# Kernel tuning notes

Measured on AMD Instinct MI355X. Metric: run time of the kernel, lower is better.

## Reference

```python
import jax, jax.numpy as jnp
import numpy as np


def setup_inputs() -> dict:
    key = jax.random.key(0)
    ks = jax.random.split(key, 6)
    B, S, D, E, F, C = 4, 2048, 1024, 8, 4096, 512
    return {
        "x": jax.random.normal(ks[0], (B, S, D), dtype=jnp.float32),
        "router": jax.random.normal(ks[1], (D, E), dtype=jnp.float32) * (1.0 / np.sqrt(D)),
        "w1": jax.random.normal(ks[2], (E, D, F), dtype=jnp.float32) * (1.0 / np.sqrt(D)),
        "b1": jnp.zeros((E, F), dtype=jnp.float32),
        "w2": jax.random.normal(ks[3], (E, F, D), dtype=jnp.float32) * (1.0 / np.sqrt(F)),
        "b2": jnp.zeros((E, D), dtype=jnp.float32),
        "capacity": C,
    }


def reference(x, router, w1, b1, w2, b2, capacity):
    # x: (B,S,D); router: (D,E); per-expert FFN weights stacked on E.
    B, S, D = x.shape
    # Gate: softmax over experts, then each expert picks its top-C tokens.
    logits = jnp.einsum('bsd,de->bse', x, router)            # (B,S,E)
    affinity = jax.nn.softmax(logits, axis=-1)               # (B,S,E)
    gating, index = jax.lax.top_k(jnp.transpose(affinity, (0, 2, 1)), capacity)  # (B,E,C)
    # Dispatch: gather token features per (expert, slot). Equivalent to the
    # one-hot einsum 'becs,bsd->becd' in the original (same math, true gather).
    x_in = jax.vmap(lambda xb, ib: xb[ib])(x, index)         # (B,E,C,D)
    # Per-expert GPT2 FFN: Linear -> GELU -> Linear (grouped GEMMs over E).
    h = jax.nn.gelu(jnp.einsum('becd,edf->becf', x_in, w1) + b1[None, :, None, :],
                    approximate=False)                        # (B,E,C,F)
    x_e = jnp.einsum('becf,efd->becd', h, w2) + b2[None, :, None, :]  # (B,E,C,D)
    # Combine: weighted scatter-add back to token positions. Equivalent to
    # einsum 'becs,bec,becd->bsd' with the one-hot dispatch mask.
    weighted = gating[..., None] * x_e                       # (B,E,C,D)
    out = jax.vmap(
        lambda ib, vb: jnp.zeros((S, D), x.dtype).at[ib.reshape(-1)].add(vb.reshape(-1, D))
    )(index, weighted)                                       # (B,S,D)
    return out
```

## Files before the change

### kernel.cpp

```cpp
#include <hip/hip_runtime.h>
#include <hip/hip_bf16.h>

#define B_ 4
#define S_ 2048
#define D_ 1024
#define E_ 8
#define F_ 4096
#define C_ 512
#define BE_ (B_*E_)

typedef __attribute__((ext_vector_type(8))) short bf16x8;
typedef __attribute__((ext_vector_type(4))) float f32x4;
typedef unsigned short u16;

static constexpr size_t OFF_AFF  = 0;
static constexpr size_t OFF_IDX  = 262144;
static constexpr size_t OFF_GATE = 327680;
static constexpr size_t OFF_XIN  = 393216;
static constexpr size_t OFF_WT1  = OFF_XIN + (size_t)BE_*C_*D_*2;
static constexpr size_t OFF_WT2  = OFF_WT1 + (size_t)E_*F_*D_*2;
static constexpr size_t OFF_H    = OFF_WT2 + (size_t)E_*D_*F_*2;
static constexpr size_t WS_NEED  = OFF_H   + (size_t)BE_*C_*F_*2;

static __device__ __forceinline__ u16 f2bf(float x) {
  __hip_bfloat16 h = __float2bfloat16(x);
  return *reinterpret_cast<u16*>(&h);
}

static __device__ __forceinline__ void gload16(const void* g, void* l) {
  __builtin_amdgcn_global_load_lds(
      (const __attribute__((address_space(1))) unsigned int*)g,
      (__attribute__((address_space(3))) unsigned int*)l, 16, 0, 0);
}

__global__ void router_kernel(const float* __restrict__ x,
                              const float* __restrict__ router,
                              float* __restrict__ aff) {
  int t = blockIdx.x;
  int b = t / S_, s = t % S_;
  int lane = threadIdx.x;
  const float* xrow = x + (size_t)t * D_;
  float acc[E_];
#pragma unroll
  for (int e = 0; e < E_; ++e) acc[e] = 0.f;
  for (int i = 0; i < D_/64; ++i) {
    int d = lane + i*64;
    float xv = xrow[d];
    const float* r = router + (size_t)d * E_;
#pragma unroll
    for (int e = 0; e < E_; ++e) acc[e] += xv * r[e];
  }
#pragma unroll
  for (int e = 0; e < E_; ++e) {
    float v = acc[e];
    for (int off = 32; off; off >>= 1) v += __shfl_down(v, off);
    acc[e] = v;
  }
  if (lane == 0) {
    float mx = acc[0];
#pragma unroll
    for (int e = 1; e < E_; ++e) mx = fmaxf(mx, acc[e]);
    float ev[E_]; float sum = 0.f;
#pragma unroll
    for (int e = 0; e < E_; ++e) { ev[e] = expf(acc[e] - mx); sum += ev[e]; }
    float inv = 1.0f / sum;
#pragma unroll
    for (int e = 0; e < E_; ++e) aff[((size_t)(b*E_ + e))*S_ + s] = ev[e]*inv;
  }
}

__global__ void topk_kernel(const float* __restrict__ aff,
                            int* __restrict__ idxb, float* __restrict__ gateb) {
  __shared__ unsigned long long keys[S_];
  int be = blockIdx.x;
  const float* a = aff + (size_t)be * S_;
  int tid = threadIdx.x;
  for (int i = tid; i < S_; i += 1024) {
    unsigned vb = __float_as_uint(a[i]);
    keys[i] = ((unsigned long long)(~vb) << 32) | (unsigned)i;
  }
  __syncthreads();
  for (int k = 2; k <= S_; k <<= 1) {
    for (int j = k >> 1; j > 0; j >>= 1) {
      for (int i = tid; i < S_; i += 1024) {
        int ixj = i ^ j;
        if (ixj > i) {
          unsigned long long ka = keys[i], kb = keys[ixj];
          bool up = ((i & k) == 0);
          if ((ka > kb) == up) { keys[i] = kb; keys[ixj] = ka; }
        }
      }
      __syncthreads();
    }
  }
  for (int c = tid; c < C_; c += 1024) {
    unsigned long long kk = keys[c];
    idxb[be*C_ + c]  = (int)(kk & 0xffffffffu);
    gateb[be*C_ + c] = __uint_as_float(~(unsigned)(kk >> 32));
  }
}

__global__ void gather_kernel(const float* __restrict__ x,
                              const int* __restrict__ idxb,
                              u16* __restrict__ x_in) {
  int rid = blockIdx.x;
  int be = rid >> 9;
  int b = be >> 3;
  int tok = idxb[rid];
  const float4* src = (const float4*)(x + ((size_t)(b * S_ + tok)) * D_);
  ushort4* dst = (ushort4*)(x_in + (size_t)rid * D_);
  int t = threadIdx.x;
#pragma unroll
  for (int i = 0; i < 2; ++i) {
    float4 v = src[t + i*128];
    ushort4 o;
    o.x = f2bf(v.x); o.y = f2bf(v.y); o.z = f2bf(v.z); o.w = f2bf(v.w);
    dst[t + i*128] = o;
  }
}

__global__ void trans_kernel(const float* __restrict__ src,
                             u16* __restrict__ dst, int RI, int RJ) {
  __shared__ float t[64][65];
  int e  = blockIdx.z;
  int j0 = blockIdx.x * 64;
  int i0 = blockIdx.y * 64;
  const float* s = src + (size_t)e * RI * RJ;
  u16* d = dst + (size_t)e * RI * RJ;
  int tid = threadIdx.x;
#pragma unroll
  for (int it = 0; it < 4; ++it) {
    int fid = it*256 + tid;
    int r = fid >> 4, c4 = fid & 15;
    float4 v = *(const float4*)(s + (size_t)(i0 + r) * RJ + j0 + c4*4);
    t[r][c4*4+0] = v.x; t[r][c4*4+1] = v.y; t[r][c4*4+2] = v.z; t[r][c4*4+3] = v.w;
  }
  __syncthreads();
#pragma unroll
  for (int it = 0; it < 4; ++it) {
    int fid = it*256 + tid;
    int rn = fid >> 4, c4 = fid & 15;
    ushort4 o;
    o.x = f2bf(t[c4*4+0][rn]); o.y = f2bf(t[c4*4+1][rn]);
    o.z = f2bf(t[c4*4+2][rn]); o.w = f2bf(t[c4*4+3][rn]);
    *(ushort4*)(d + (size_t)(j0 + rn) * RI + i0 + c4*4) = o;
  }
}

template<int EPI, int N, int K, int NBLK>
__global__ __launch_bounds__(256, 4)
void gemm_kernel(const u16* __restrict__ A, const u16* __restrict__ Bt,
                 const float* __restrict__ bias, void* __restrict__ outp,
                 const int* __restrict__ idxb, const float* __restrict__ gateb,
                 float* __restrict__ dout) {
  __shared__ __align__(16) char lds[32768];
  char* ldsA = lds;
  char* ldsB = lds + 16384;
  const int tid  = threadIdx.x;
  const int wave = tid >> 6, lane = tid & 63;

  const int bid = blockIdx.x;
  const int e   = bid & 7;
  const int r   = bid >> 3;
  const int nb  = r % NBLK;
  const int rm  = r / NBLK;
  const int mb  = rm & 3;
  const int b   = rm >> 2;
  const int be  = b * E_ + e;
  const int m0  = mb * 128;
  const int n0  = nb * 128;

  const u16* Ab = A  + (size_t)be * C_ * K + (size_t)m0 * K;
  const u16* Bb = Bt + (size_t)e  * N  * K + (size_t)n0 * K;

  f32x4 acc[4][4];
#pragma unroll
  for (int i = 0; i < 4; ++i)
#pragma unroll
    for (int j = 0; j < 4; ++j) acc[i][j] = (f32x4){0.f,0.f,0.f,0.f};

  const int wr = wave >> 1, wc = wave & 1;
  const int chi = lane >> 4;
  const int l15 = lane & 15;

  for (int kt = 0; kt < K/64; ++kt) {
    const int k0 = kt * 64;
#pragma unroll
    for (int i = 0; i < 4; ++i) {
      int slot = i*256 + tid;
      int row = slot >> 3, c = slot & 7;
      int sc = (c ^ (row & 7)) << 3;
      gload16(Ab + (size_t)row * K + k0 + sc, ldsA + (i*256 + wave*64)*16);
      gload16(Bb + (size_t)row * K + k0 + sc, ldsB + (i*256 + wave*64)*16);
    }
    __syncthreads();
    bf16x8 af[2][4], bfr[2][4];
#pragma unroll
    for (int kk = 0; kk < 2; ++kk) {
#pragma unroll
      for (int mi = 0; mi < 4; ++mi) {
        int row = wr*64 + mi*16 + l15;
        int ch  = kk*4 + chi;
        af[kk][mi] = *(const bf16x8*)(ldsA + row*128 + (((ch ^ (row & 7)) << 4)));
        int rowb = wc*64 + mi*16 + l15;
        bfr[kk][mi] = *(const bf16x8*)(ldsB + rowb*128 + (((ch ^ (rowb & 7)) << 4)));
      }
    }
#pragma unroll
    for (int kk = 0; kk < 2; ++kk)
#pragma unroll
      for (int mi = 0; mi < 4; ++mi)
#pragma unroll
        for (int ni = 0; ni < 4; ++ni)
          acc[mi][ni] = __builtin_amdgcn_mfma_f32_16x16x32_bf16(
              af[kk][mi], bfr[kk][ni], acc[mi][ni], 0, 0, 0);
    __syncthreads();
  }

  const int r4 = lane >> 4;
  if (EPI == 0) {
    __hip_bfloat16* hb = (__hip_bfloat16*)outp + (size_t)be * C_ * N;
    const float* bias_e = bias + e * N;
#pragma unroll
    for (int mi = 0; mi < 4; ++mi) {
#pragma unroll
      for (int j = 0; j < 4; ++j) {
        int row = m0 + wr*64 + mi*16 + r4*4 + j;
        __hip_bfloat16* hrow = hb + (size_t)row * N;
#pragma unroll
        for (int ni = 0; ni < 4; ++ni) {
          int col = n0 + wc*64 + ni*16 + l15;
          float v = acc[mi][ni][j] + bias_e[col];
          float g = 0.5f * v * (1.0f + erff(v * 0.70710678118654752f));
          hrow[col] = __float2bfloat16(g);
        }
      }
    }
  } else {
    const float* bias_e = bias + e * N;
    int bb = be >> 3;
#pragma unroll
    for (int mi = 0; mi < 4; ++mi) {
#pragma unroll
      for (int j = 0; j < 4; ++j) {
        int rowl = m0 + wr*64 + mi*16 + r4*4 + j;
        int tok = idxb[be*C_ + rowl];
        float gt = gateb[be*C_ + rowl];
        float* orow = dout + ((size_t)bb * S_ + tok) * (size_t)D_;
#pragma unroll
        for (int ni = 0; ni < 4; ++ni) {
          int col = n0 + wc*64 + ni*16 + l15;
          float v = (acc[mi][ni][j] + bias_e[col]) * gt;
          atomicAdd(orow + col, v);
        }
      }
    }
  }
}

extern "C" void kernel_launch(void* const* d_in, const int* in_sizes, int n_in,
                              void* d_out, int out_size, void* d_ws, size_t ws_size,
                              hipStream_t stream) {
  const float* x      = (const float*)d_in[0];
  const float* router = (const float*)d_in[1];
  const float* w1     = (const float*)d_in[2];
  const float* b1     = (const float*)d_in[3];
  const float* w2     = (const float*)d_in[4];
  const float* b2     = (const float*)d_in[5];
  float* out = (float*)d_out;

  if (ws_size < WS_NEED) return;

  char* ws = (char*)d_ws;
  float* aff   = (float*)(ws + OFF_AFF);
  int*   idxb  = (int*)(ws + OFF_IDX);
  float* gateb = (float*)(ws + OFF_GATE);
  u16*   x_in  = (u16*)(ws + OFF_XIN);
  u16*   wt1   = (u16*)(ws + OFF_WT1);
  u16*   wt2   = (u16*)(ws + OFF_WT2);
  u16*   h     = (u16*)(ws + OFF_H);

  router_kernel<<<B_*S_, 64, 0, stream>>>(x, router, aff);
  topk_kernel<<<BE_, 1024, 0, stream>>>(aff, idxb, gateb);
  gather_kernel<<<BE_*C_, 128, 0, stream>>>(x, idxb, x_in);
  trans_kernel<<<dim3(F_/64, D_/64, E_), 256, 0, stream>>>(w1, wt1, D_, F_);
  trans_kernel<<<dim3(D_/64, F_/64, E_), 256, 0, stream>>>(w2, wt2, F_, D_);
  hipMemsetAsync(d_out, 0, (size_t)out_size * sizeof(float), stream);

  gemm_kernel<0, F_, D_, F_/128><<<E_*(F_/128)*4*B_, 256, 0, stream>>>(
      x_in, wt1, b1, (void*)h, nullptr, nullptr, nullptr);
  gemm_kernel<1, D_, F_, D_/128><<<E_*(D_/128)*4*B_, 256, 0, stream>>>(
      h, wt2, b2, nullptr, idxb, gateb, out);
}
```

Before: 483.9 us.

## Rewrite expert GEMMs as 256x256 8-wave double-buffered pipelined kernel

Replaces the 128x128 single-buffered GEMM with a 256x256-tile, 512-thread kernel that uses 128KB of LDS for double buffering. Global-to-LDS loads for the next K tiles are interleaved with four MFMA phases, and manual waitcnt, barriers and setprio are used to overlap memory with compute. The larger tile raises arithmetic intensity per LDS byte and hides load latency. In exchange it lowers occupancy, leaves fewer blocks for the D-output GEMM (256 blocks), and relies on fragile hand-tuned synchronisation.

```diff
diff --git a/kernel.cpp b/kernel.cpp
--- a/kernel.cpp
+++ b/kernel.cpp
@@ -12,6 +12,8 @@
 typedef __attribute__((ext_vector_type(8))) short bf16x8;
 typedef __attribute__((ext_vector_type(4))) float f32x4;
 typedef unsigned short u16;
+
+#define MFMA16 __builtin_amdgcn_mfma_f32_16x16x32_bf16
 
 static constexpr size_t OFF_AFF  = 0;
 static constexpr size_t OFF_IDX  = 262144;
@@ -148,88 +150,164 @@
 }
 
 template<int EPI, int N, int K, int NBLK>
-__global__ __launch_bounds__(256, 4)
-void gemm_kernel(const u16* __restrict__ A, const u16* __restrict__ Bt,
-                 const float* __restrict__ bias, void* __restrict__ outp,
-                 const int* __restrict__ idxb, const float* __restrict__ gateb,
-                 float* __restrict__ dout) {
-  __shared__ __align__(16) char lds[32768];
-  char* ldsA = lds;
-  char* ldsB = lds + 16384;
+__global__ __launch_bounds__(512, 2)
+void gemm8_kernel(const u16* __restrict__ A, const u16* __restrict__ Bt,
+                  const float* __restrict__ bias, void* __restrict__ outp,
+                  const int* __restrict__ idxb, const float* __restrict__ gateb,
+                  float* __restrict__ dout) {
+  constexpr int NT = K / 64;
+  __shared__ __align__(16) char lds[131072];
   const int tid  = threadIdx.x;
   const int wave = tid >> 6, lane = tid & 63;
+  const int wm = wave >> 2, wn = wave & 3;
+  const int l15 = lane & 15, chi = lane >> 4;
 
   const int bid = blockIdx.x;
   const int e   = bid & 7;
   const int r   = bid >> 3;
   const int nb  = r % NBLK;
   const int rm  = r / NBLK;
-  const int mb  = rm & 3;
-  const int b   = rm >> 2;
+  const int mb  = rm & 1;
+  const int b   = rm >> 1;
   const int be  = b * E_ + e;
-  const int m0  = mb * 128;
-  const int n0  = nb * 128;
-
-  const u16* Ab = A  + (size_t)be * C_ * K + (size_t)m0 * K;
-  const u16* Bb = Bt + (size_t)e  * N  * K + (size_t)n0 * K;
-
-  f32x4 acc[4][4];
-#pragma unroll
-  for (int i = 0; i < 4; ++i)
+  const int m0  = mb * 256;
+  const int n0  = nb * 256;
+
+  const u16* Ab  = A  + (size_t)be * C_ * K + (size_t)m0 * K;
+  const u16* Bb  = Bt + (size_t)e  * N  * K + (size_t)n0 * K;
+  const u16* Ab2 = Ab + (size_t)128 * K;
+  const u16* Bb2 = Bb + (size_t)128 * K;
+
+  const int sr = tid >> 3, scn = tid & 7;
+  const size_t off0 = (size_t)sr * K + (size_t)((scn ^ (sr & 7)) << 3);
+  const size_t off1 = off0 + (size_t)64 * K;
+  const int ldsd = tid * 16;
+
+#define STAGE(tt, so, gb) \
+  if ((tt) < NT) { \
+    const u16* g_ = (gb) + (size_t)(tt) * 64; \
+    char* l_ = lds + (((tt) & 1) * 65536) + (so); \
+    gload16(g_ + off0, l_ + ldsd); \
+    gload16(g_ + off1, l_ + 8192 + ldsd); \
+  }
+
+  const int q7  = l15 & 7;
+  const int ch0 = ((chi    ) ^ q7) << 4;
+  const int ch1 = ((4 + chi) ^ q7) << 4;
+  const int aoff = wm * 16384 + l15 * 128;
+  const int boff = 32768 + (wn >> 1) * 16384 + (wn & 1) * 8192 + l15 * 128;
+
+  f32x4 acc[8][4];
+#pragma unroll
+  for (int i = 0; i < 8; ++i)
 #pragma unroll
     for (int j = 0; j < 4; ++j) acc[i][j] = (f32x4){0.f,0.f,0.f,0.f};
 
-  const int wr = wave >> 1, wc = wave & 1;
-  const int chi = lane >> 4;
-  const int l15 = lane & 15;
-
-  for (int kt = 0; kt < K/64; ++kt) {
-    const int k0 = kt * 64;
-#pragma unroll
-    for (int i = 0; i < 4; ++i) {
-      int slot = i*256 + tid;
-      int row = slot >> 3, c = slot & 7;
-      int sc = (c ^ (row & 7)) << 3;
-      gload16(Ab + (size_t)row * K + k0 + sc, ldsA + (i*256 + wave*64)*16);
-      gload16(Bb + (size_t)row * K + k0 + sc, ldsB + (i*256 + wave*64)*16);
-    }
-    __syncthreads();
-    bf16x8 af[2][4], bfr[2][4];
-#pragma unroll
-    for (int kk = 0; kk < 2; ++kk) {
-#pragma unroll
-      for (int mi = 0; mi < 4; ++mi) {
-        int row = wr*64 + mi*16 + l15;
-        int ch  = kk*4 + chi;
-        af[kk][mi] = *(const bf16x8*)(ldsA + row*128 + (((ch ^ (row & 7)) << 4)));
-        int rowb = wc*64 + mi*16 + l15;
-        bfr[kk][mi] = *(const bf16x8*)(ldsB + rowb*128 + (((ch ^ (rowb & 7)) << 4)));
-      }
-    }
-#pragma unroll
-    for (int kk = 0; kk < 2; ++kk)
-#pragma unroll
-      for (int mi = 0; mi < 4; ++mi)
-#pragma unroll
-        for (int ni = 0; ni < 4; ++ni)
-          acc[mi][ni] = __builtin_amdgcn_mfma_f32_16x16x32_bf16(
-              af[kk][mi], bfr[kk][ni], acc[mi][ni], 0, 0, 0);
-    __syncthreads();
-  }
+  STAGE(0, 0,     Ab);
+  STAGE(0, 16384, Ab2);
+  STAGE(0, 32768, Bb);
+  STAGE(0, 49152, Bb2);
+  STAGE(1, 32768, Bb);
+  STAGE(1, 49152, Bb2);
+  asm volatile("s_waitcnt vmcnt(4)" ::: "memory");
+  __builtin_amdgcn_s_barrier();
+
+  bf16x8 af[2][4], bA[2][2], bB[2][2];
+  for (int t = 0; t < NT; ++t) {
+    const char* cb = lds + (t & 1) * 65536;
+#pragma unroll
+    for (int m = 0; m < 4; ++m) {
+      af[0][m] = *(const bf16x8*)(cb + aoff + m*2048 + ch0);
+      af[1][m] = *(const bf16x8*)(cb + aoff + m*2048 + ch1);
+    }
+#pragma unroll
+    for (int n = 0; n < 2; ++n) {
+      bA[0][n] = *(const bf16x8*)(cb + boff + n*2048 + ch0);
+      bA[1][n] = *(const bf16x8*)(cb + boff + n*2048 + ch1);
+    }
+    STAGE(t+1, 0, Ab);
+    asm volatile("s_waitcnt lgkmcnt(8)" ::: "memory");
+    __builtin_amdgcn_s_barrier();
+    asm volatile("s_waitcnt lgkmcnt(0)" ::: "memory");
+    __builtin_amdgcn_s_setprio(1);
+#pragma unroll
+    for (int m = 0; m < 4; ++m)
+#pragma unroll
+      for (int n = 0; n < 2; ++n) {
+        acc[m][n] = MFMA16(af[0][m], bA[0][n], acc[m][n], 0, 0, 0);
+        acc[m][n] = MFMA16(af[1][m], bA[1][n], acc[m][n], 0, 0, 0);
+      }
+    __builtin_amdgcn_s_setprio(0);
+    __builtin_amdgcn_s_barrier();
+#pragma unroll
+    for (int n = 0; n < 2; ++n) {
+      bB[0][n] = *(const bf16x8*)(cb + boff + (2+n)*2048 + ch0);
+      bB[1][n] = *(const bf16x8*)(cb + boff + (2+n)*2048 + ch1);
+    }
+    STAGE(t+1, 16384, Ab2);
+    __builtin_amdgcn_s_barrier();
+    asm volatile("s_waitcnt lgkmcnt(0)" ::: "memory");
+    __builtin_amdgcn_s_setprio(1);
+#pragma unroll
+    for (int m = 0; m < 4; ++m)
+#pragma unroll
+      for (int n = 0; n < 2; ++n) {
+        acc[m][2+n] = MFMA16(af[0][m], bB[0][n], acc[m][2+n], 0, 0, 0);
+        acc[m][2+n] = MFMA16(af[1][m], bB[1][n], acc[m][2+n], 0, 0, 0);
+      }
+    __builtin_amdgcn_s_setprio(0);
+    __builtin_amdgcn_s_barrier();
+#pragma unroll
+    for (int m = 0; m < 4; ++m) {
+      af[0][m] = *(const bf16x8*)(cb + aoff + (4+m)*2048 + ch0);
+      af[1][m] = *(const bf16x8*)(cb + aoff + (4+m)*2048 + ch1);
+    }
+    STAGE(t+2, 32768, Bb);
+    __builtin_amdgcn_s_barrier();
+    asm volatile("s_waitcnt lgkmcnt(0)" ::: "memory");
+    __builtin_amdgcn_s_setprio(1);
+#pragma unroll
+    for (int m = 0; m < 4; ++m)
+#pragma unroll
+      for (int n = 0; n < 2; ++n) {
+        acc[4+m][2+n] = MFMA16(af[0][m], bB[0][n], acc[4+m][2+n], 0, 0, 0);
+        acc[4+m][2+n] = MFMA16(af[1][m], bB[1][n], acc[4+m][2+n], 0, 0, 0);
+      }
+    __builtin_amdgcn_s_setprio(0);
+    __builtin_amdgcn_s_barrier();
+    STAGE(t+2, 49152, Bb2);
+    if (t < NT-2) {
+      asm volatile("s_waitcnt vmcnt(4)" ::: "memory");
+    } else if (t == NT-2) {
+      asm volatile("s_waitcnt vmcnt(0)" ::: "memory");
+    }
+    __builtin_amdgcn_s_barrier();
+    __builtin_amdgcn_s_setprio(1);
+#pragma unroll
+    for (int m = 0; m < 4; ++m)
+#pragma unroll
+      for (int n = 0; n < 2; ++n) {
+        acc[4+m][n] = MFMA16(af[0][m], bA[0][n], acc[4+m][n], 0, 0, 0);
+        acc[4+m][n] = MFMA16(af[1][m], bA[1][n], acc[4+m][n], 0, 0, 0);
+      }
+    __builtin_amdgcn_s_setprio(0);
+    __builtin_amdgcn_s_barrier();
+  }
+#undef STAGE
 
   const int r4 = lane >> 4;
   if (EPI == 0) {
     __hip_bfloat16* hb = (__hip_bfloat16*)outp + (size_t)be * C_ * N;
     const float* bias_e = bias + e * N;
 #pragma unroll
-    for (int mi = 0; mi < 4; ++mi) {
+    for (int mi = 0; mi < 8; ++mi) {
 #pragma unroll
       for (int j = 0; j < 4; ++j) {
-        int row = m0 + wr*64 + mi*16 + r4*4 + j;
+        int row = m0 + wm*128 + mi*16 + r4*4 + j;
         __hip_bfloat16* hrow = hb + (size_t)row * N;
 #pragma unroll
         for (int ni = 0; ni < 4; ++ni) {
-          int col = n0 + wc*64 + ni*16 + l15;
+          int col = n0 + wn*64 + ni*16 + l15;
           float v = acc[mi][ni][j] + bias_e[col];
           float g = 0.5f * v * (1.0f + erff(v * 0.70710678118654752f));
           hrow[col] = __float2bfloat16(g);
@@ -240,16 +318,16 @@
     const float* bias_e = bias + e * N;
     int bb = be >> 3;
 #pragma unroll
-    for (int mi = 0; mi < 4; ++mi) {
+    for (int mi = 0; mi < 8; ++mi) {
 #pragma unroll
       for (int j = 0; j < 4; ++j) {
-        int rowl = m0 + wr*64 + mi*16 + r4*4 + j;
+        int rowl = m0 + wm*128 + mi*16 + r4*4 + j;
         int tok = idxb[be*C_ + rowl];
         float gt = gateb[be*C_ + rowl];
         float* orow = dout + ((size_t)bb * S_ + tok) * (size_t)D_;
 #pragma unroll
         for (int ni = 0; ni < 4; ++ni) {
-          int col = n0 + wc*64 + ni*16 + l15;
+          int col = n0 + wn*64 + ni*16 + l15;
           float v = (acc[mi][ni][j] + bias_e[col]) * gt;
           atomicAdd(orow + col, v);
         }
@@ -287,8 +365,8 @@
   trans_kernel<<<dim3(D_/64, F_/64, E_), 256, 0, stream>>>(w2, wt2, F_, D_);
   hipMemsetAsync(d_out, 0, (size_t)out_size * sizeof(float), stream);
 
-  gemm_kernel<0, F_, D_, F_/128><<<E_*(F_/128)*4*B_, 256, 0, stream>>>(
+  gemm8_kernel<0, F_, D_, F_/256><<<E_*(F_/256)*2*B_, 512, 0, stream>>>(
       x_in, wt1, b1, (void*)h, nullptr, nullptr, nullptr);
-  gemm_kernel<1, D_, F_, D_/128><<<E_*(D_/128)*4*B_, 256, 0, stream>>>(
+  gemm8_kernel<1, D_, F_, D_/256><<<E_*(D_/256)*2*B_, 512, 0, stream>>>(
       h, wt2, b2, nullptr, idxb, gateb, out);
 }
```

After: 492.3 us. No clear change (+1.7%).
